# Performance work log

Measured on AMD Instinct MI355X. Metric: run time of the kernel, lower is better.

Reference implementation:

```python
import jax, jax.numpy as jnp
import numpy as np
from jax import lax

BN_EPS = 1e-5
HEADS = 2


def dw_conv(x, w, stride, pad):
    # depthwise conv, NCHW, weight OIHW with I=1, groups=C
    return lax.conv_general_dilated(
        x, w, (stride, stride), [(pad, pad), (pad, pad)],
        dimension_numbers=('NCHW', 'OIHW', 'NCHW'),
        feature_group_count=x.shape[1])


def bn(x, g, b, m, v):
    inv = g * lax.rsqrt(v + BN_EPS)
    return (x - m[:, None, None]) * inv[:, None, None] + b[:, None, None]


def conv1x1(x, w, b):
    return jnp.einsum('bchw,oc->bohw', x, w) + b[:, None, None]


def setup_inputs() -> dict:
    key = jax.random.key(0)
    ks = jax.random.split(key, 20)
    B, C, H, W = 32, 128, 56, 56
    r = lambda i, shape, s=0.05: jax.random.normal(ks[i], shape, jnp.float32) * s
    return {
        'x': jax.random.normal(ks[0], (B, C, H, W), jnp.float32),
        'q_w': r(1, (C, C)), 'q_b': r(2, (C,)),
        'kv_w': r(3, (2 * C, C)), 'kv_b': r(4, (2 * C,)),
        'sr1_w': r(5, (C, 1, 4, 4), 0.2),
        'sr1_g': jax.random.uniform(ks[6], (C,), jnp.float32) + 0.5,
        'sr1_b': r(7, (C,)),
        'sr1_m': r(8, (C,)),
        'sr1_v': jax.random.uniform(ks[9], (C,), jnp.float32) + 0.5,
        'sr2_w': r(10, (C, 1, 1, 1), 0.5),
        'sr2_g': jax.random.uniform(ks[11], (C,), jnp.float32) + 0.5,
        'sr2_b': r(12, (C,)),
        'sr2_m': r(13, (C,)),
        'sr2_v': jax.random.uniform(ks[14], (C,), jnp.float32) + 0.5,
        'local_w': r(15, (C, 1, 3, 3), 0.2), 'local_b': r(16, (C,)),
    }


def reference(x, q_w, q_b, kv_w, kv_b,
              sr1_w, sr1_g, sr1_b, sr1_m, sr1_v,
              sr2_w, sr2_g, sr2_b, sr2_m, sr2_v,
              local_w, local_b):
    B, C, H, W = x.shape
    h = HEADS
    d = C // h
    scale = d ** -0.5

    # q projection: 1x1 conv -> [B, h, N, d]
    q = conv1x1(x, q_w, q_b)
    q = q.reshape(B, h, d, H * W).transpose(0, 1, 3, 2)

    # spatial reduction: depthwise strided conv + BN + ReLU, then depthwise 1x1 + BN
    kv = jax.nn.relu(bn(dw_conv(x, sr1_w, 4, 2), sr1_g, sr1_b, sr1_m, sr1_v))
    kv = bn(kv * sr2_w.reshape(C, 1, 1), sr2_g, sr2_b, sr2_m, sr2_v)

    # depthwise 3x3 local conv + residual
    kv = dw_conv(kv, local_w, 1, 1) + local_b[:, None, None] + kv

    # kv projection and split
    kvp = conv1x1(kv, kv_w, kv_b)
    k, v = jnp.split(kvp, 2, axis=1)
    Nk = k.shape[2] * k.shape[3]
    k = k.reshape(B, h, d, Nk)                       # [B,h,d,Nk]
    v = v.reshape(B, h, d, Nk).transpose(0, 1, 3, 2)  # [B,h,Nk,d]

    attn = jax.nn.softmax(jnp.einsum('bhnd,bhdm->bhnm', q, k) * scale, axis=-1)
    out = jnp.einsum('bhnm,bhmd->bhnd', attn, v)      # [B,h,N,d]
    return out.transpose(0, 1, 3, 2).reshape(B, C, H, W)
```

## Files before the change

kernel.cpp:

```cpp
#include <hip/hip_runtime.h>
#include <hip/hip_bf16.h>

#define B_    32
#define C_    128
#define H_    56
#define W_    56
#define N_    3136
#define HK_   15
#define NK_   225
#define D_    64
#define SCL_  0.1803368801111731f

typedef __attribute__((ext_vector_type(8))) short bf16x8;
typedef __attribute__((ext_vector_type(4))) float f32x4;

__device__ __forceinline__ float b2f(unsigned short u) {
    union { float f; unsigned int i; } x;
    x.i = ((unsigned int)u) << 16;
    return x.f;
}
__device__ __forceinline__ unsigned short f2b(float f) {
    __hip_bfloat16 h = __float2bfloat16(f);
    return *(unsigned short*)&h;
}
__device__ __forceinline__ unsigned int cvtpk(float a, float b) {
    unsigned int r;
    asm("v_cvt_pk_bf16_f32 %0, %1, %2" : "=v"(r) : "v"(a), "v"(b));
    return r;
}
__device__ __forceinline__ float exp2a(float x) {
    float r;
    asm("v_exp_f32 %0, %1" : "=v"(r) : "v"(x));
    return r;
}

__device__ __forceinline__ void gll16(const char* g, char* l) {
    __builtin_amdgcn_global_load_lds(
        (const __attribute__((address_space(1))) unsigned int*)g,
        (__attribute__((address_space(3))) unsigned int*)l,
        16, 0, 0);
}

__global__ __launch_bounds__(256) void prep_kernel(
        const float* __restrict__ x,
        const float* __restrict__ sr1_w, const float* __restrict__ sr1_g,
        const float* __restrict__ sr1_b, const float* __restrict__ sr1_m,
        const float* __restrict__ sr1_v, const float* __restrict__ sr2_w,
        const float* __restrict__ sr2_g, const float* __restrict__ sr2_b,
        const float* __restrict__ sr2_m, const float* __restrict__ sr2_v,
        const float* __restrict__ local_w, const float* __restrict__ local_b,
        const float* __restrict__ q_w, const float* __restrict__ q_b,
        const float* __restrict__ kv_w, const float* __restrict__ kv_b,
        float* __restrict__ kv2,
        unsigned short* __restrict__ wkq_sw, unsigned short* __restrict__ wv_sw,
        float* __restrict__ kwb, float* __restrict__ wb, float* __restrict__ qkb) {
    int tid = threadIdx.x;
    __shared__ union {
        struct { float xim[H_ * W_]; float kvt[HK_][HK_ + 1]; } sr;
        float wq[64][16];
    } U;

    if (blockIdx.x >= (unsigned)(B_ * C_)) {
        int bx = blockIdx.x - B_ * C_;
        int h  = bx >> 3, cg = bx & 7;
        for (int idx = tid; idx < 64 * 16; idx += 256)
            U.wq[idx >> 4][idx & 15] =
                q_w[(size_t)(h * 64 + (idx >> 4)) * 128 + cg * 16 + (idx & 15)];
        __syncthreads();
        {
            int cl = tid >> 4;
            int c  = cg * 16 + cl;
            int cp0 = (tid & 15) * 8;
            float acc[8];
#pragma unroll
            for (int i = 0; i < 8; ++i) acc[i] = 0.f;
            for (int e = 0; e < 64; ++e) {
                float wqv = U.wq[e][cl];
                const float* wkrow = kv_w + (size_t)(h * 64 + e) * 128 + cp0;
#pragma unroll
                for (int i = 0; i < 8; ++i) acc[i] += wqv * wkrow[i];
            }
            char* base = (char*)wkq_sw + (size_t)h * 32768 + (size_t)c * 256;
            ushort4 u0, u1;
            u0.x = f2b(acc[0] * SCL_); u0.y = f2b(acc[1] * SCL_);
            u0.z = f2b(acc[2] * SCL_); u0.w = f2b(acc[3] * SCL_);
            u1.x = f2b(acc[4] * SCL_); u1.y = f2b(acc[5] * SCL_);
            u1.z = f2b(acc[6] * SCL_); u1.w = f2b(acc[7] * SCL_);
            int sw = (c & 7) << 4;
            *(ushort4*)(base + ((cp0 * 2) ^ sw)) = u0;
            *(ushort4*)(base + ((cp0 * 2 + 8) ^ sw)) = u1;
        }
        if (tid < 16) {
            int cl = tid, c = cg * 16 + cl;
            float s = 0.f;
            for (int e = 0; e < 64; ++e) s += kv_b[h * 64 + e] * U.wq[e][cl];
            kwb[h * 128 + c] = s * SCL_;
        }
        if (cg == 0) {
            if (tid < 128) {
                float s = 0.f;
                for (int e = 0; e < 64; ++e)
                    s += q_b[h * 64 + e] * kv_w[(size_t)(h * 64 + e) * 128 + tid];
                wb[h * 128 + tid] = s * SCL_;
            }
            if (tid == 0) {
                float s = 0.f;
                for (int e = 0; e < 64; ++e) s += q_b[h * 64 + e] * kv_b[h * 64 + e];
                qkb[h] = s * SCL_;
            }
        }
        if (cg == 1) {
            for (int idx = tid; idx < 64 * 128; idx += 256) {
                int e = idx >> 7, cp = idx & 127;
                unsigned short val = f2b(kv_w[(size_t)(128 + h * 64 + e) * 128 + cp]);
                *(unsigned short*)((char*)wv_sw + (size_t)h * 16384 + (size_t)e * 256 +
                                   (((cp * 2) ^ ((e & 7) << 4)))) = val;
            }
        }
        return;
    }

    int bc = blockIdx.x;
    int c  = bc & (C_ - 1);
    const float* xp = x + (size_t)bc * (H_ * W_);
    for (int idx = tid; idx < (H_ * W_) / 4; idx += 256)
        ((float4*)U.sr.xim)[idx] = ((const float4*)xp)[idx];
    __syncthreads();

    int p = tid;
    int oy = p / HK_, ox = p % HK_;
    if (p < NK_) {
        float s = 0.f;
#pragma unroll
        for (int ky = 0; ky < 4; ++ky) {
            int iy = oy * 4 - 2 + ky;
            if (iy < 0 || iy >= H_) continue;
#pragma unroll
            for (int kx = 0; kx < 4; ++kx) {
                int ix = ox * 4 - 2 + kx;
                if (ix < 0 || ix >= W_) continue;
                s += U.sr.xim[iy * W_ + ix] * sr1_w[c * 16 + ky * 4 + kx];
            }
        }
        float inv1 = sr1_g[c] * rsqrtf(sr1_v[c] + 1e-5f);
        s = (s - sr1_m[c]) * inv1 + sr1_b[c];
        s = fmaxf(s, 0.f);
        s *= sr2_w[c];
        float inv2 = sr2_g[c] * rsqrtf(sr2_v[c] + 1e-5f);
        s = (s - sr2_m[c]) * inv2 + sr2_b[c];
        U.sr.kvt[oy][ox] = s;
    }
    __syncthreads();
    if (p < NK_) {
        float v = U.sr.kvt[oy][ox] + local_b[c];
#pragma unroll
        for (int dy = -1; dy <= 1; ++dy) {
            int yy = oy + dy;
            if (yy < 0 || yy >= HK_) continue;
#pragma unroll
            for (int dx = -1; dx <= 1; ++dx) {
                int xx = ox + dx;
                if (xx < 0 || xx >= HK_) continue;
                v += U.sr.kvt[yy][xx] * local_w[c * 9 + (dy + 1) * 3 + (dx + 1)];
            }
        }
        kv2[(size_t)bc * NK_ + p] = v;
    }
}

#define L2B(r, cb) ((r) * 256 + ((cb) ^ (((r) & 7) << 4)))
__global__ __launch_bounds__(256, 2) void kvw_kernel(
        const float* __restrict__ kv2,
        const float* __restrict__ kv_b,
        const unsigned short* __restrict__ wkq_sw,
        const unsigned short* __restrict__ wv_sw,
        const float* __restrict__ kwb,
        const float* __restrict__ wb,
        const float* __restrict__ qkb,
        unsigned short* __restrict__ kw,
        float* __restrict__ bias_s,
        unsigned short* __restrict__ vbuf) {
    int b = blockIdx.x, h = blockIdx.y, mh = blockIdx.z;
    int bh = b * 2 + h;
    int m0 = mh * 64;
    int tid = threadIdx.x;
    int lo = tid & 15, hi = (tid >> 4) & 3, wid = tid >> 6;

    __shared__ char K2[16384];
    __shared__ char WQ[32768];
    __shared__ char WV[16384];

    {
        const char* srcQ = (const char*)wkq_sw + (size_t)h * 32768 + tid * 16;
        char* dstQ = WQ + wid * 1024;
#pragma unroll
        for (int i = 0; i < 8; ++i) gll16(srcQ + i * 4096, dstQ + i * 4096);
        const char* srcV = (const char*)wv_sw + (size_t)h * 16384 + tid * 16;
        char* dstV = WV + wid * 1024;
#pragma unroll
        for (int i = 0; i < 4; ++i) gll16(srcV + i * 4096, dstV + i * 4096);
    }
    {
        int j = tid & 63;
        int mg = m0 + j;
        bool val = (mg < NK_);
#pragma unroll
        for (int it = 0; it < 8; ++it) {
            int c0 = (tid >> 6) * 4 + it * 16;
            ushort4 u;
            if (val) {
                const float* kp = kv2 + ((size_t)b * 128 + c0) * NK_ + mg;
                u.x = f2b(kp[0]);
                u.y = f2b(kp[NK_]);
                u.z = f2b(kp[2 * NK_]);
                u.w = f2b(kp[3 * NK_]);
            } else { u.x = 0; u.y = 0; u.z = 0; u.w = 0; }
            *(ushort4*)(K2 + L2B(j, c0 * 2)) = u;
        }
    }
    __syncthreads();

    bf16x8 aq[4];
#pragma unroll
    for (int ks = 0; ks < 4; ++ks)
        aq[ks] = *(const bf16x8*)(K2 + L2B(wid * 16 + lo, ks * 64 + hi * 16));

    char* kwB = (char*)kw + (size_t)bh * 65536;
#pragma unroll
    for (int ct = 0; ct < 8; ++ct) {
        f32x4 acc = {0.f, 0.f, 0.f, 0.f};
#pragma unroll
        for (int ks = 0; ks < 4; ++ks) {
            bf16x8 bq = *(const bf16x8*)(WQ + L2B(ct * 16 + lo, ks * 64 + hi * 16));
            acc = __builtin_amdgcn_mfma_f32_16x16x32_bf16(aq[ks], bq, acc, 0, 0, 0);
        }
        int c = ct * 16 + lo;
        float kb = kwb[h * 128 + c];
#pragma unroll
        for (int r = 0; r < 4; ++r) {
            int mg = m0 + wid * 16 + hi * 4 + r;
            *(unsigned short*)(kwB + (size_t)mg * 256 + (((c * 2) ^ ((mg & 7) << 4)))) =
                f2b(acc[r] + kb);
        }
    }

    char* vB = (char*)vbuf + (size_t)bh * 32768;
#pragma unroll
    for (int et = 0; et < 4; ++et) {
        f32x4 acc = {0.f, 0.f, 0.f, 0.f};
#pragma unroll
        for (int ks = 0; ks < 4; ++ks) {
            bf16x8 bv = *(const bf16x8*)(WV + L2B(et * 16 + lo, ks * 64 + hi * 16));
            acc = __builtin_amdgcn_mfma_f32_16x16x32_bf16(aq[ks], bv, acc, 0, 0, 0);
        }
        int e = et * 16 + lo;
        float vb = kv_b[128 + h * 64 + e];
#pragma unroll
        for (int r = 0; r < 4; ++r) {
            int mg = m0 + wid * 16 + hi * 4 + r;
            *(unsigned short*)(vB + (size_t)e * 512 + (((mg * 2) ^ ((e & 7) << 4)))) =
                f2b(acc[r] + vb);
        }
    }

    if (tid < 64) {
        int mg = m0 + tid;
        float s;
        if (mg >= NK_) s = -1e30f;
        else {
            s = qkb[h];
            for (int i = 0; i < 128; ++i) {
                int cp = (i + (tid & 7) * 16) & 127;
                s += b2f(*(const unsigned short*)(K2 + L2B(tid, cp * 2))) * wb[h * 128 + cp];
            }
        }
        bias_s[(size_t)bh * 256 + mg] = s;
    }
}

#define KWB(rl, cb) ((rl) * 256 + ((cb) ^ (((rl) & 7) << 4)))
#define CVB(e, cb)  ((e) * 512 + ((cb) ^ (((e) & 7) << 4)))

__global__ __launch_bounds__(256, 3) void attn_kernel(
        const float* __restrict__ x,
        const unsigned short* __restrict__ kw,
        const float* __restrict__ bias_s,
        const unsigned short* __restrict__ vbuf,
        float* __restrict__ out) {
    int flat = blockIdx.x;
    int xcd  = flat & 7;
    int idx  = flat >> 3;
    int g    = idx / 49;
    int jt   = idx % 49;
    int bh   = g * 8 + xcd;
    int bb   = bh >> 1;
    int h    = bh & 1;
    int n0   = jt * 64;
    int tid = threadIdx.x;
    int lo  = tid & 15;
    int hi  = (tid >> 4) & 3;
    int wid = tid >> 6;
    int jw  = wid * 16;

    __shared__ char LA[16384];
    __shared__ char LC[32768];
    __shared__ float LBIAS[256];

    const char* kwG = (const char*)kw + (size_t)bh * 65536;
    const char* vG  = (const char*)vbuf + (size_t)bh * 32768;

    const float* xb = x + ((size_t)bb * 128) * N_ + n0 + jw + lo;
    float xf[4][8];
#pragma unroll
    for (int ks = 0; ks < 4; ++ks) {
#pragma unroll
        for (int i = 0; i < 8; ++i)
            xf[ks][i] = xb[(size_t)(ks * 32 + hi * 8 + i) * N_];
    }
    __builtin_amdgcn_sched_barrier(0);

    {
        if (wid == 0)
            gll16((const char*)(bias_s + (size_t)bh * 256) + tid * 16, (char*)LBIAS);
        const char* s0 = kwG + tid * 16;
        char* d0 = LA + wid * 1024;
        gll16(s0, d0); gll16(s0 + 4096, d0 + 4096);
        const char* s1 = kwG + 8192 + tid * 16;
        char* d1 = LA + 8192 + wid * 1024;
        gll16(s1, d1); gll16(s1 + 4096, d1 + 4096);
        const char* sc = vG + tid * 16;
        char* dc = LC + wid * 1024;
#pragma unroll
        for (int i = 0; i < 8; ++i) gll16(sc + i * 4096, dc + i * 4096);
    }

    bf16x8 aq[4];
#pragma unroll
    for (int ks = 0; ks < 4; ++ks) {
        uint4 u;
        u.x = cvtpk(xf[ks][0], xf[ks][1]);
        u.y = cvtpk(xf[ks][2], xf[ks][3]);
        u.z = cvtpk(xf[ks][4], xf[ks][5]);
        u.w = cvtpk(xf[ks][6], xf[ks][7]);
        aq[ks] = *(bf16x8*)&u;
    }

    asm volatile("s_waitcnt vmcnt(10)" ::: "memory");
    __builtin_amdgcn_s_barrier();
    __builtin_amdgcn_sched_barrier(0);

    f32x4 s[15];
#pragma unroll
    for (int t = 0; t < 8; ++t) {
        char* Bt = LA + (t & 1) * 8192;
#pragma unroll
        for (int ml = 0; ml < 2; ++ml) {
            int mt = t * 2 + ml;
            if (mt >= 15) continue;
            f32x4 acc = *(const f32x4*)&LBIAS[mt * 16 + hi * 4];
#pragma unroll
            for (int ks = 0; ks < 4; ++ks) {
                bf16x8 bk = *(const bf16x8*)(Bt + KWB(ml * 16 + lo, ks * 64 + hi * 16));
                acc = __builtin_amdgcn_mfma_f32_16x16x32_bf16(bk, aq[ks], acc, 0, 0, 0);
            }
            s[mt] = acc;
        }
        if (t < 6) {
            __builtin_amdgcn_s_barrier();
            const char* sn = kwG + (t + 2) * 8192 + tid * 16;
            char* dn = LA + (t & 1) * 8192 + wid * 1024;
            gll16(sn, dn); gll16(sn + 4096, dn + 4096);
        }
        if (t < 7) {
            if (t == 0)      asm volatile("s_waitcnt vmcnt(10)" ::: "memory");
            else if (t < 6)  asm volatile("s_waitcnt vmcnt(2)" ::: "memory");
            else             asm volatile("s_waitcnt vmcnt(0)" ::: "memory");
            __builtin_amdgcn_s_barrier();
            __builtin_amdgcn_sched_barrier(0);
        }
    }

    float mxv = s[0][0];
#pragma unroll
    for (int mt = 0; mt < 15; ++mt) {
#pragma unroll
        for (int r = 0; r < 4; ++r) mxv = fmaxf(mxv, s[mt][r]);
    }
    mxv = fmaxf(mxv, __shfl_xor(mxv, 16));
    mxv = fmaxf(mxv, __shfl_xor(mxv, 32));
    float smv = 0.f;
#pragma unroll
    for (int mt = 0; mt < 15; ++mt) {
#pragma unroll
        for (int r = 0; r < 4; ++r) {
            float pe = exp2a(s[mt][r] - mxv);
            s[mt][r] = pe;
            smv += pe;
        }
    }
    smv += __shfl_xor(smv, 16);
    smv += __shfl_xor(smv, 32);
    float rinv = 1.f / smv;

    bf16x8 bp[8];
    int sA = lo + (hi & 1) * 32;
    int sB = sA + 16;
    bool lowm = (hi < 2);
#pragma unroll
    for (int ks = 0; ks < 8; ++ks) {
        int t0 = 2 * ks, t1 = 2 * ks + 1;
        unsigned int a0 = cvtpk(s[t0][0], s[t0][1]);
        unsigned int a1 = cvtpk(s[t0][2], s[t0][3]);
        unsigned int r0A = (unsigned int)__shfl((int)a0, sA);
        unsigned int r1A = (unsigned int)__shfl((int)a1, sA);
        unsigned int r0B = (unsigned int)__shfl((int)a0, sB);
        unsigned int r1B = (unsigned int)__shfl((int)a1, sB);
        unsigned int dw0, dw1, dw2, dw3;
        if (ks < 7) {
            unsigned int b0 = cvtpk(s[t1][0], s[t1][1]);
            unsigned int b1 = cvtpk(s[t1][2], s[t1][3]);
            unsigned int q0A = (unsigned int)__shfl((int)b0, sA);
            unsigned int q1A = (unsigned int)__shfl((int)b1, sA);
            unsigned int q0B = (unsigned int)__shfl((int)b0, sB);
            unsigned int q1B = (unsigned int)__shfl((int)b1, sB);
            dw0 = lowm ? r0A : q0A;
            dw1 = lowm ? r1A : q1A;
            dw2 = lowm ? r0B : q0B;
            dw3 = lowm ? r1B : q1B;
        } else {
            dw0 = lowm ? r0A : 0u;
            dw1 = lowm ? r1A : 0u;
            dw2 = lowm ? r0B : 0u;
            dw3 = lowm ? r1B : 0u;
        }
        uint4 d4 = {dw0, dw1, dw2, dw3};
        bp[ks] = *(bf16x8*)&d4;
    }

#pragma unroll
    for (int et = 0; et < 4; ++et) {
        f32x4 acc = {0.f, 0.f, 0.f, 0.f};
#pragma unroll
        for (int ks = 0; ks < 8; ++ks) {
            bf16x8 av = *(const bf16x8*)(LC + CVB(et * 16 + lo, ks * 64 + hi * 16));
            acc = __builtin_amdgcn_mfma_f32_16x16x32_bf16(av, bp[ks], acc, 0, 0, 0);
        }
        int e = et * 16 + hi * 4;
#pragma unroll
        for (int r = 0; r < 4; ++r)
            out[((size_t)bb * 128 + h * 64 + e + r) * N_ + n0 + jw + lo] = acc[r] * rinv;
    }
}

extern "C" void kernel_launch(void* const* d_in, const int* in_sizes, int n_in,
                              void* d_out, int out_size, void* d_ws, size_t ws_size,
                              hipStream_t stream) {
    const float* x       = (const float*)d_in[0];
    const float* q_w     = (const float*)d_in[1];
    const float* q_b     = (const float*)d_in[2];
    const float* kv_w    = (const float*)d_in[3];
    const float* kv_b    = (const float*)d_in[4];
    const float* sr1_w   = (const float*)d_in[5];
    const float* sr1_g   = (const float*)d_in[6];
    const float* sr1_b   = (const float*)d_in[7];
    const float* sr1_m   = (const float*)d_in[8];
    const float* sr1_v   = (const float*)d_in[9];
    const float* sr2_w   = (const float*)d_in[10];
    const float* sr2_g   = (const float*)d_in[11];
    const float* sr2_b   = (const float*)d_in[12];
    const float* sr2_m   = (const float*)d_in[13];
    const float* sr2_v   = (const float*)d_in[14];
    const float* local_w = (const float*)d_in[15];
    const float* local_b = (const float*)d_in[16];

    char* ws = (char*)d_ws;
    float* kv2              = (float*)(ws + 0);
    unsigned short* wkq_sw  = (unsigned short*)(ws + 3686400);
    unsigned short* wv_sw   = (unsigned short*)(ws + 3751936);
    unsigned short* kw      = (unsigned short*)(ws + 3784704);
    unsigned short* vbuf    = (unsigned short*)(ws + 7979008);
    float* bias_s           = (float*)(ws + 10076160);
    float* kwb              = (float*)(ws + 10141696);
    float* wb               = (float*)(ws + 10142720);
    float* qkb              = (float*)(ws + 10143744);

    prep_kernel<<<B_ * C_ + 16, 256, 0, stream>>>(
        x, sr1_w, sr1_g, sr1_b, sr1_m, sr1_v,
        sr2_w, sr2_g, sr2_b, sr2_m, sr2_v, local_w, local_b,
        q_w, q_b, kv_w, kv_b,
        kv2, wkq_sw, wv_sw, kwb, wb, qkb);
    kvw_kernel<<<dim3(B_, 2, 4), 256, 0, stream>>>(
        kv2, kv_b, wkq_sw, wv_sw, kwb, wb, qkb, kw, bias_s, vbuf);
    attn_kernel<<<3136, 256, 0, stream>>>(
        x, kw, bias_s, vbuf, (float*)d_out);
}
```

Before: 86.28 us.

## Double attention tile to 128 queries per 512-thread block, read prep input directly

The attention kernel now uses 512-thread blocks covering 128 query positions, so each block's K and V loads from global memory into LDS are shared by twice as many queries and the grid shrinks from 3136 to 1600 blocks. The ragged last tile is handled with clamped loads and masked stores, and the async copy counts and waitcnt values are adjusted to match. The MFMA loops are wrapped in s_setprio raises, and the softmax max reduction is restructured into a tree. The prep kernel no longer stages the whole 56x56 input plane in LDS and instead reads strided taps straight from global memory. This cuts LDS use and a barrier there, but the partly redundant global reads now depend on the cache.

```diff
diff --git a/kernel.cpp b/kernel.cpp
--- a/kernel.cpp
+++ b/kernel.cpp
@@ -55,16 +55,14 @@
         unsigned short* __restrict__ wkq_sw, unsigned short* __restrict__ wv_sw,
         float* __restrict__ kwb, float* __restrict__ wb, float* __restrict__ qkb) {
     int tid = threadIdx.x;
-    __shared__ union {
-        struct { float xim[H_ * W_]; float kvt[HK_][HK_ + 1]; } sr;
-        float wq[64][16];
-    } U;
+    __shared__ float kvt[HK_][HK_ + 1];
+    __shared__ float wq[64][16];
 
     if (blockIdx.x >= (unsigned)(B_ * C_)) {
         int bx = blockIdx.x - B_ * C_;
         int h  = bx >> 3, cg = bx & 7;
         for (int idx = tid; idx < 64 * 16; idx += 256)
-            U.wq[idx >> 4][idx & 15] =
+            wq[idx >> 4][idx & 15] =
                 q_w[(size_t)(h * 64 + (idx >> 4)) * 128 + cg * 16 + (idx & 15)];
         __syncthreads();
         {
@@ -75,7 +73,7 @@
 #pragma unroll
             for (int i = 0; i < 8; ++i) acc[i] = 0.f;
             for (int e = 0; e < 64; ++e) {
-                float wqv = U.wq[e][cl];
+                float wqv = wq[e][cl];
                 const float* wkrow = kv_w + (size_t)(h * 64 + e) * 128 + cp0;
 #pragma unroll
                 for (int i = 0; i < 8; ++i) acc[i] += wqv * wkrow[i];
@@ -93,7 +91,7 @@
         if (tid < 16) {
             int cl = tid, c = cg * 16 + cl;
             float s = 0.f;
-            for (int e = 0; e < 64; ++e) s += kv_b[h * 64 + e] * U.wq[e][cl];
+            for (int e = 0; e < 64; ++e) s += kv_b[h * 64 + e] * wq[e][cl];
             kwb[h * 128 + c] = s * SCL_;
         }
         if (cg == 0) {
@@ -123,10 +121,6 @@
     int bc = blockIdx.x;
     int c  = bc & (C_ - 1);
     const float* xp = x + (size_t)bc * (H_ * W_);
-    for (int idx = tid; idx < (H_ * W_) / 4; idx += 256)
-        ((float4*)U.sr.xim)[idx] = ((const float4*)xp)[idx];
-    __syncthreads();
-
     int p = tid;
     int oy = p / HK_, ox = p % HK_;
     if (p < NK_) {
@@ -139,7 +133,7 @@
             for (int kx = 0; kx < 4; ++kx) {
                 int ix = ox * 4 - 2 + kx;
                 if (ix < 0 || ix >= W_) continue;
-                s += U.sr.xim[iy * W_ + ix] * sr1_w[c * 16 + ky * 4 + kx];
+                s += xp[iy * W_ + ix] * sr1_w[c * 16 + ky * 4 + kx];
             }
         }
         float inv1 = sr1_g[c] * rsqrtf(sr1_v[c] + 1e-5f);
@@ -148,11 +142,11 @@
         s *= sr2_w[c];
         float inv2 = sr2_g[c] * rsqrtf(sr2_v[c] + 1e-5f);
         s = (s - sr2_m[c]) * inv2 + sr2_b[c];
-        U.sr.kvt[oy][ox] = s;
+        kvt[oy][ox] = s;
     }
     __syncthreads();
     if (p < NK_) {
-        float v = U.sr.kvt[oy][ox] + local_b[c];
+        float v = kvt[oy][ox] + local_b[c];
 #pragma unroll
         for (int dy = -1; dy <= 1; ++dy) {
             int yy = oy + dy;
@@ -161,7 +155,7 @@
             for (int dx = -1; dx <= 1; ++dx) {
                 int xx = ox + dx;
                 if (xx < 0 || xx >= HK_) continue;
-                v += U.sr.kvt[yy][xx] * local_w[c * 9 + (dy + 1) * 3 + (dx + 1)];
+                v += kvt[yy][xx] * local_w[c * 9 + (dy + 1) * 3 + (dx + 1)];
             }
         }
         kv2[(size_t)bc * NK_ + p] = v;
@@ -281,7 +275,7 @@
 #define KWB(rl, cb) ((rl) * 256 + ((cb) ^ (((rl) & 7) << 4)))
 #define CVB(e, cb)  ((e) * 512 + ((cb) ^ (((e) & 7) << 4)))
 
-__global__ __launch_bounds__(256, 3) void attn_kernel(
+__global__ __launch_bounds__(512, 6) void attn_kernel(
         const float* __restrict__ x,
         const unsigned short* __restrict__ kw,
         const float* __restrict__ bias_s,
@@ -290,12 +284,12 @@
     int flat = blockIdx.x;
     int xcd  = flat & 7;
     int idx  = flat >> 3;
-    int g    = idx / 49;
-    int jt   = idx % 49;
+    int g    = idx / 25;
+    int jt   = idx % 25;
     int bh   = g * 8 + xcd;
     int bb   = bh >> 1;
     int h    = bh & 1;
-    int n0   = jt * 64;
+    int n0   = jt * 128;
     int tid = threadIdx.x;
     int lo  = tid & 15;
     int hi  = (tid >> 4) & 3;
@@ -309,7 +303,10 @@
     const char* kwG = (const char*)kw + (size_t)bh * 65536;
     const char* vG  = (const char*)vbuf + (size_t)bh * 32768;
 
-    const float* xb = x + ((size_t)bb * 128) * N_ + n0 + jw + lo;
+    int jv = n0 + jw + lo;
+    bool jok = (jv < N_);
+    int jc = jok ? jv : (N_ - 1);
+    const float* xb = x + ((size_t)bb * 128) * N_ + jc;
     float xf[4][8];
 #pragma unroll
     for (int ks = 0; ks < 4; ++ks) {
@@ -322,16 +319,11 @@
     {
         if (wid == 0)
             gll16((const char*)(bias_s + (size_t)bh * 256) + tid * 16, (char*)LBIAS);
-        const char* s0 = kwG + tid * 16;
-        char* d0 = LA + wid * 1024;
-        gll16(s0, d0); gll16(s0 + 4096, d0 + 4096);
-        const char* s1 = kwG + 8192 + tid * 16;
-        char* d1 = LA + 8192 + wid * 1024;
-        gll16(s1, d1); gll16(s1 + 4096, d1 + 4096);
-        const char* sc = vG + tid * 16;
-        char* dc = LC + wid * 1024;
-#pragma unroll
-        for (int i = 0; i < 8; ++i) gll16(sc + i * 4096, dc + i * 4096);
+        gll16(kwG + tid * 16,        LA + wid * 1024);
+        gll16(kwG + 8192 + tid * 16, LA + 8192 + wid * 1024);
+#pragma unroll
+        for (int i = 0; i < 4; ++i)
+            gll16(vG + i * 8192 + tid * 16, LC + i * 8192 + wid * 1024);
     }
 
     bf16x8 aq[4];
@@ -345,7 +337,7 @@
         aq[ks] = *(bf16x8*)&u;
     }
 
-    asm volatile("s_waitcnt vmcnt(10)" ::: "memory");
+    asm volatile("s_waitcnt vmcnt(5)" ::: "memory");
     __builtin_amdgcn_s_barrier();
     __builtin_amdgcn_sched_barrier(0);
 
@@ -353,6 +345,7 @@
 #pragma unroll
     for (int t = 0; t < 8; ++t) {
         char* Bt = LA + (t & 1) * 8192;
+        __builtin_amdgcn_s_setprio(1);
 #pragma unroll
         for (int ml = 0; ml < 2; ++ml) {
             int mt = t * 2 + ml;
@@ -365,26 +358,27 @@
             }
             s[mt] = acc;
         }
+        __builtin_amdgcn_s_setprio(0);
         if (t < 6) {
             __builtin_amdgcn_s_barrier();
-            const char* sn = kwG + (t + 2) * 8192 + tid * 16;
-            char* dn = LA + (t & 1) * 8192 + wid * 1024;
-            gll16(sn, dn); gll16(sn + 4096, dn + 4096);
+            gll16(kwG + (t + 2) * 8192 + tid * 16, LA + (t & 1) * 8192 + wid * 1024);
         }
         if (t < 7) {
-            if (t == 0)      asm volatile("s_waitcnt vmcnt(10)" ::: "memory");
-            else if (t < 6)  asm volatile("s_waitcnt vmcnt(2)" ::: "memory");
-            else             asm volatile("s_waitcnt vmcnt(0)" ::: "memory");
+            if (t < 6) asm volatile("s_waitcnt vmcnt(1)" ::: "memory");
+            else       asm volatile("s_waitcnt vmcnt(0)" ::: "memory");
             __builtin_amdgcn_s_barrier();
             __builtin_amdgcn_sched_barrier(0);
         }
     }
 
-    float mxv = s[0][0];
-#pragma unroll
-    for (int mt = 0; mt < 15; ++mt) {
-#pragma unroll
-        for (int r = 0; r < 4; ++r) mxv = fmaxf(mxv, s[mt][r]);
+    float mxv = fmaxf(fmaxf(s[0][0], s[0][1]), fmaxf(s[0][2], s[0][3]));
+#pragma unroll
+    for (int mt = 1; mt < 15; mt += 2) {
+        float a = fmaxf(fmaxf(s[mt][0], s[mt][1]), fmaxf(s[mt][2], s[mt][3]));
+        float b = (mt + 1 < 15)
+            ? fmaxf(fmaxf(s[mt + 1][0], s[mt + 1][1]), fmaxf(s[mt + 1][2], s[mt + 1][3]))
+            : a;
+        mxv = fmaxf(mxv, fmaxf(a, b));
     }
     mxv = fmaxf(mxv, __shfl_xor(mxv, 16));
     mxv = fmaxf(mxv, __shfl_xor(mxv, 32));
@@ -440,15 +434,19 @@
 #pragma unroll
     for (int et = 0; et < 4; ++et) {
         f32x4 acc = {0.f, 0.f, 0.f, 0.f};
+        __builtin_amdgcn_s_setprio(1);
 #pragma unroll
         for (int ks = 0; ks < 8; ++ks) {
             bf16x8 av = *(const bf16x8*)(LC + CVB(et * 16 + lo, ks * 64 + hi * 16));
             acc = __builtin_amdgcn_mfma_f32_16x16x32_bf16(av, bp[ks], acc, 0, 0, 0);
         }
+        __builtin_amdgcn_s_setprio(0);
         int e = et * 16 + hi * 4;
-#pragma unroll
-        for (int r = 0; r < 4; ++r)
-            out[((size_t)bb * 128 + h * 64 + e + r) * N_ + n0 + jw + lo] = acc[r] * rinv;
+        if (jok) {
+#pragma unroll
+            for (int r = 0; r < 4; ++r)
+                out[((size_t)bb * 128 + h * 64 + e + r) * N_ + jv] = acc[r] * rinv;
+        }
     }
 }
 
@@ -491,6 +489,6 @@
         kv2, wkq_sw, wv_sw, kwb, wb, qkb);
     kvw_kernel<<<dim3(B_, 2, 4), 256, 0, stream>>>(
         kv2, kv_b, wkq_sw, wv_sw, kwb, wb, qkb, kw, bias_s, vbuf);
-    attn_kernel<<<3136, 256, 0, stream>>>(
+    attn_kernel<<<1600, 512, 0, stream>>>(
         x, kw, bias_s, vbuf, (float*)d_out);
 }
```

Result: slower. 107.1 us (+24.1%).
